# Kernel tuning notes

Measured on AMD Instinct MI355X. Metric: run time of the kernel, lower is better.

The kernel has to match this reference:

```python
import jax, jax.numpy as jnp
import numpy as np

B, LS, LL = 1024, 128, 2048
E, VOCAB = 16, 160000
NH, KD = 8, 6
LSH_DIM, TOPK = 16, 48
D_ITEM = 3 * E  # 48
EPS = 1e-3  # keras LayerNormalization default epsilon


def setup_inputs() -> dict:
    key = jax.random.key(0)
    ks = iter(jax.random.split(key, 64))
    def nk():
        return next(ks)
    def ids(shape):
        return jax.random.randint(nk(), shape, 0, VOCAB, dtype=jnp.int32)
    inp = {}
    for n in ['uid', 'utag1', 'utag2', 'utag3', 'utag4',
              'label_goods_ids', 'label_shop_ids', 'label_cate_ids']:
        inp[n] = ids((B,))
    for n in ['shortterm_goods_ids', 'shortterm_shop_ids', 'shortterm_cate_ids']:
        inp[n] = ids((B, LS))
    for n in ['longterm_goods_ids', 'longterm_shop_ids', 'longterm_cate_ids']:
        inp[n] = ids((B, LL))
    def rn(shape, s=0.05):
        return (jax.random.normal(nk(), shape) * s).astype(jnp.float32)
    inp['emb_table'] = rn((VOCAB, E))
    inp['H'] = rn((D_ITEM, LSH_DIM), 1.0)  # non-trainable random projection
    for p in ('s', 'l'):
        inp[p + 'Wq'] = rn((D_ITEM, NH, KD)); inp[p + 'bq'] = jnp.zeros((NH, KD), jnp.float32)
        inp[p + 'Wk'] = rn((D_ITEM, NH, KD)); inp[p + 'bk'] = jnp.zeros((NH, KD), jnp.float32)
        inp[p + 'Wv'] = rn((D_ITEM, NH, KD)); inp[p + 'bv'] = jnp.zeros((NH, KD), jnp.float32)
        inp[p + 'Wo'] = rn((NH, KD, D_ITEM)); inp[p + 'bo'] = jnp.zeros((D_ITEM,), jnp.float32)
    Din = D_ITEM + 5 * E + D_ITEM + D_ITEM  # 224
    inp['W1'] = rn((Din, 200)); inp['b1'] = jnp.zeros((200,), jnp.float32)
    inp['g1'] = jnp.ones((200,), jnp.float32); inp['be1'] = jnp.zeros((200,), jnp.float32)
    inp['W2'] = rn((200, 80)); inp['b2'] = jnp.zeros((80,), jnp.float32)
    inp['g2'] = jnp.ones((80,), jnp.float32); inp['be2'] = jnp.zeros((80,), jnp.float32)
    inp['W3'] = rn((80, 1)); inp['b3'] = jnp.zeros((1,), jnp.float32)
    return inp


def _ln(x, g, b):
    m = jnp.mean(x, axis=-1, keepdims=True)
    v = jnp.mean((x - m) ** 2, axis=-1, keepdims=True)
    return (x - m) * jax.lax.rsqrt(v + EPS) * g + b


def _mha(q, kv, mask3, Wq, bq, Wk, bk, Wv, bv, Wo, bo):
    # q: [B,1,D], kv: [B,K,D], mask3: [B,1,K] float (1=keep)
    qh = jnp.einsum('bqe,ehd->bqhd', q, Wq) + bq
    kh = jnp.einsum('bke,ehd->bkhd', kv, Wk) + bk
    vh = jnp.einsum('bke,ehd->bkhd', kv, Wv) + bv
    sc = jnp.einsum('bqhd,bkhd->bhqk', qh, kh) / jnp.sqrt(jnp.float32(KD))
    sc = sc + (1.0 - mask3[:, None, :, :]) * jnp.float32(-1e9)
    a = jax.nn.softmax(sc, axis=-1)
    o = jnp.einsum('bhqk,bkhd->bqhd', a, vh)
    return jnp.einsum('bqhd,hde->bqe', o, Wo) + bo


def reference(uid, utag1, utag2, utag3, utag4,
              label_goods_ids, label_shop_ids, label_cate_ids,
              shortterm_goods_ids, shortterm_shop_ids, shortterm_cate_ids,
              longterm_goods_ids, longterm_shop_ids, longterm_cate_ids,
              emb_table, H,
              sWq, sbq, sWk, sbk, sWv, sbv, sWo, sbo,
              lWq, lbq, lWk, lbk, lWv, lbv, lWo, lbo,
              W1, b1, g1, be1, W2, b2, g2, be2, W3, b3):
    short_mask = shortterm_goods_ids == 0  # padding_index == 0
    long_mask = longterm_goods_ids == 0

    def stack_embed(lst):
        X = jnp.stack([t if t.ndim == 2 else t[:, None] for t in lst], axis=2)  # [B,L,F]
        Xe = emb_table[X]  # [B,L,F,E]
        return Xe.reshape(Xe.shape[0], Xe.shape[1], -1)

    X_item = stack_embed([label_goods_ids, label_shop_ids, label_cate_ids])  # [B,1,48]
    X_user = stack_embed([uid, utag1, utag2, utag3, utag4])                  # [B,1,80]
    X_short = stack_embed([shortterm_goods_ids, shortterm_shop_ids, shortterm_cate_ids])  # [B,LS,48]
    X_long = stack_embed([longterm_goods_ids, longterm_shop_ids, longterm_cate_ids])      # [B,LL,48]

    # short-term interest
    slen = jnp.sum((~short_mask).astype(jnp.int32), axis=1)
    smask = (jnp.arange(LS)[None, :] < slen[:, None]).astype(jnp.float32)[:, None, :]
    short_int = _mha(X_item, X_short, smask, sWq, sbq, sWk, sbk, sWv, sbv, sWo, sbo)[:, 0]

    # long-term interest: LSH sign-hash hamming top-k retrieval
    series_codes = jnp.sign(jnp.einsum('ble,em->blm', X_long, H))  # [B,LL,16]
    item_codes = jnp.sign(jnp.einsum('ble,em->blm', X_item, H))    # [B,1,16]
    scores = jnp.sum((series_codes == item_codes).astype(jnp.float32), axis=-1)  # [B,LL]
    scores = jnp.where(long_mask, -jnp.inf, scores)
    _, idx = jax.lax.top_k(scores, TOPK)  # descending, padded entries last
    top_emb = jnp.take_along_axis(X_long, idx[:, :, None], axis=1)  # [B,TOPK,48]
    top_mask = jnp.take_along_axis(long_mask, idx, axis=1)
    llen = jnp.sum((~top_mask).astype(jnp.int32), axis=1)
    lmask = (jnp.arange(TOPK)[None, :] < llen[:, None]).astype(jnp.float32)[:, None, :]
    long_int = _mha(X_item, top_emb, lmask, lWq, lbq, lWk, lbk, lWv, lbv, lWo, lbo)[:, 0]

    x = jnp.concatenate([X_item[:, 0], X_user[:, 0], short_int, long_int], axis=1)  # [B,224]
    h1 = jax.nn.relu(_ln(x @ W1 + b1, g1, be1))
    h2 = jax.nn.relu(_ln(h1 @ W2 + b2, g2, be2))
    out = jax.nn.sigmoid(h2 @ W3 + b3)  # [B,1]
    return out
```

## Files before the change

### kernel.cpp

```cpp
#include <hip/hip_runtime.h>
#include <math.h>

#define BB 1024
#define LSx 128
#define LLx 2048
#define TOPKx 48

__global__ __launch_bounds__(256) void k_score(
    const int* __restrict__ lg, const int* __restrict__ lsh, const int* __restrict__ lc,
    const int* __restrict__ ig, const int* __restrict__ ish, const int* __restrict__ ici,
    const float* __restrict__ emb, const float* __restrict__ Hm,
    signed char* __restrict__ gsc)
{
  __shared__ float Xitem[48];
  __shared__ int icode[16];
  const int b = blockIdx.y, tid = threadIdx.x;

  if (tid < 48) {
    const int seg = tid >> 4, e = tid & 15;
    const int id = (seg == 0) ? ig[b] : (seg == 1) ? ish[b] : ici[b];
    Xitem[tid] = emb[(size_t)id * 16 + e];
  }
  __syncthreads();
  if (tid < 16) {
    float dd = 0.f;
    for (int e = 0; e < 48; ++e) dd += Xitem[e] * Hm[e * 16 + tid];
    icode[tid] = (dd > 0.f) ? 1 : (dd < 0.f ? -1 : 0);
  }
  __syncthreads();

  const int l = blockIdx.x * 256 + tid;
  const size_t off = (size_t)b * LLx + l;
  const int gid = lg[off];
  int sc;
  if (gid == 0) {
    sc = -1;
  } else {
    const int sid = lsh[off], cid = lc[off];
    float d[16];
    #pragma unroll
    for (int m = 0; m < 16; ++m) d[m] = 0.f;
    const int ids3[3] = {gid, sid, cid};
    #pragma unroll
    for (int seg = 0; seg < 3; ++seg) {
      const float* row = emb + (size_t)ids3[seg] * 16;
      const float4 r0 = ((const float4*)row)[0];
      const float4 r1 = ((const float4*)row)[1];
      const float4 r2 = ((const float4*)row)[2];
      const float4 r3 = ((const float4*)row)[3];
      const float x[16] = {r0.x, r0.y, r0.z, r0.w, r1.x, r1.y, r1.z, r1.w,
                           r2.x, r2.y, r2.z, r2.w, r3.x, r3.y, r3.z, r3.w};
      const float* hb = Hm + seg * 256;
      #pragma unroll
      for (int i = 0; i < 16; ++i) {
        const float xi = x[i];
        #pragma unroll
        for (int mc = 0; mc < 4; ++mc) {
          const float4 h4 = *(const float4*)(hb + i * 16 + mc * 4);
          d[mc * 4 + 0] += xi * h4.x;
          d[mc * 4 + 1] += xi * h4.y;
          d[mc * 4 + 2] += xi * h4.z;
          d[mc * 4 + 3] += xi * h4.w;
        }
      }
    }
    sc = 0;
    #pragma unroll
    for (int m = 0; m < 16; ++m) {
      const int cs = (d[m] > 0.f) ? 1 : (d[m] < 0.f ? -1 : 0);
      sc += (cs == icode[m]) ? 1 : 0;
    }
  }
  gsc[off] = (signed char)sc;
}

template<int K, int STRIDE, bool IS_LONG>
__global__ __launch_bounds__(128) void k_mha(
    const int* __restrict__ kg, const int* __restrict__ ks, const int* __restrict__ kc,
    const int* __restrict__ ig, const int* __restrict__ ish, const int* __restrict__ ici,
    const float* __restrict__ emb,
    const float* __restrict__ Wq, const float* __restrict__ bq,
    const float* __restrict__ Wk, const float* __restrict__ bk,
    const float* __restrict__ Wv, const float* __restrict__ bv,
    const float* __restrict__ Wo, const float* __restrict__ bo,
    const int* __restrict__ sel,
    float* __restrict__ outv)
{
  __shared__ float Xitem[48];
  __shared__ float qh[48];
  __shared__ __align__(16) float vhs[K][48];
  __shared__ float scs[8][K + 4];
  __shared__ float osm[48];
  __shared__ unsigned char validf[K];
  const int b = blockIdx.x, tid = threadIdx.x;

  if (tid < 48) {
    const int seg = tid >> 4, e = tid & 15;
    const int id = (seg == 0) ? ig[b] : (seg == 1) ? ish[b] : ici[b];
    Xitem[tid] = emb[(size_t)id * 16 + e];
  }
  __syncthreads();
  if (tid < 48) {
    float a = bq[tid];
    for (int e = 0; e < 48; ++e) a += Xitem[e] * Wq[e * 48 + tid];
    qh[tid] = a;
  }

  int gid = 0, sid = 0, cid = 0;
  if (tid < K) {
    const int pos = IS_LONG ? sel[b * TOPKx + tid] : tid;
    const size_t off = (size_t)b * STRIDE + pos;
    gid = kg[off]; sid = ks[off]; cid = kc[off];
  }
  const int nval = __syncthreads_count((tid < K) && (gid != 0));

  if (tid < K) {
    validf[tid] = IS_LONG ? (unsigned char)(gid != 0) : (unsigned char)(tid < nval);
    float kh[48], vh[48];
    #pragma unroll
    for (int j = 0; j < 48; ++j) { kh[j] = bk[j]; vh[j] = bv[j]; }
    const int ids3[3] = {gid, sid, cid};
    #pragma unroll
    for (int seg = 0; seg < 3; ++seg) {
      const float* row = emb + (size_t)ids3[seg] * 16;
      #pragma unroll
      for (int i4 = 0; i4 < 4; ++i4) {
        const float4 xv = ((const float4*)row)[i4];
        const float xs[4] = {xv.x, xv.y, xv.z, xv.w};
        #pragma unroll
        for (int c = 0; c < 4; ++c) {
          const int e = seg * 16 + i4 * 4 + c;
          const float* wkr = Wk + e * 48;
          const float* wvr = Wv + e * 48;
          const float xe = xs[c];
          #pragma unroll
          for (int j = 0; j < 48; ++j) {
            kh[j] += xe * wkr[j];
            vh[j] += xe * wvr[j];
          }
        }
      }
    }
    #pragma unroll
    for (int h = 0; h < 8; ++h) {
      float s = 0.f;
      #pragma unroll
      for (int d = 0; d < 6; ++d) s += qh[h * 6 + d] * kh[h * 6 + d];
      scs[h][tid] = s * 0.40824829046386301637f;
    }
    #pragma unroll
    for (int j = 0; j < 48; ++j) vhs[tid][j] = vh[j];
  }
  __syncthreads();

  {
    const int h = tid >> 4, l16 = tid & 15;
    float amax = -INFINITY;
    for (int k = l16; k < K; k += 16) if (validf[k]) amax = fmaxf(amax, scs[h][k]);
    #pragma unroll
    for (int m = 1; m < 16; m <<= 1) amax = fmaxf(amax, __shfl_xor(amax, m, 16));
    if (nval == 0) {
      for (int k = l16; k < K; k += 16) scs[h][k] = 1.0f / (float)K;
    } else {
      float ssum = 0.f;
      for (int k = l16; k < K; k += 16) {
        const float ev = validf[k] ? expf(scs[h][k] - amax) : 0.f;
        scs[h][k] = ev;
        ssum += ev;
      }
      #pragma unroll
      for (int m = 1; m < 16; m <<= 1) ssum += __shfl_xor(ssum, m, 16);
      const float inv = 1.0f / ssum;
      for (int k = l16; k < K; k += 16) scs[h][k] *= inv;
    }
  }
  __syncthreads();

  if (tid < 48) {
    const int h = tid / 6;
    float a = 0.f;
    for (int k = 0; k < K; ++k) a += scs[h][k] * vhs[k][tid];
    osm[tid] = a;
  }
  __syncthreads();
  if (tid < 48) {
    float r = bo[tid];
    for (int j = 0; j < 48; ++j) r += osm[j] * Wo[j * 48 + tid];
    outv[b * 48 + tid] = r;
  }
}

__global__ __launch_bounds__(256) void k_mha_long(
    const int* __restrict__ kg, const int* __restrict__ ks, const int* __restrict__ kc,
    const int* __restrict__ ig, const int* __restrict__ ish, const int* __restrict__ ici,
    const float* __restrict__ emb,
    const float* __restrict__ Wq, const float* __restrict__ bq,
    const float* __restrict__ Wk, const float* __restrict__ bk,
    const float* __restrict__ Wv, const float* __restrict__ bv,
    const float* __restrict__ Wo, const float* __restrict__ bo,
    const signed char* __restrict__ gsc,
    float* __restrict__ outv)
{
  __shared__ int hist[18];
  __shared__ int cnt_above;
  __shared__ int wsum[4];
  __shared__ int selsh[TOPKx];
  __shared__ float Xitem[48];
  __shared__ float qh[48];
  __shared__ __align__(16) float vhs[TOPKx][48];
  __shared__ float scs[8][TOPKx + 4];
  __shared__ float osm[48];
  __shared__ unsigned char validf[TOPKx];
  const int b = blockIdx.x, tid = threadIdx.x;

  const int2 myv = ((const int2*)(gsc + (size_t)b * LLx))[tid];
  signed char loc[8];
  *(int2*)loc = myv;

  if (tid < 18) hist[tid] = 0;
  if (tid == 0) cnt_above = 0;
  if (tid < 48) {
    const int seg = tid >> 4, e = tid & 15;
    const int id = (seg == 0) ? ig[b] : (seg == 1) ? ish[b] : ici[b];
    Xitem[tid] = emb[(size_t)id * 16 + e];
  }
  __syncthreads();

  #pragma unroll
  for (int j = 0; j < 8; ++j) atomicAdd(&hist[(int)loc[j] + 1], 1);
  if (tid < 48) {
    float a = bq[tid];
    for (int e = 0; e < 48; ++e) a += Xitem[e] * Wq[e * 48 + tid];
    qh[tid] = a;
  }
  __syncthreads();

  int above = 0, tval = -1, need = 0;
  for (int s = 16; s >= -1; --s) {
    const int c = hist[s + 1];
    if (above + c >= TOPKx) { tval = s; need = TOPKx - above; break; }
    above += c;
  }

  const int base_l = tid * (LLx / 256);
  int cnt = 0;
  #pragma unroll
  for (int j = 0; j < 8; ++j) cnt += ((int)loc[j] == tval) ? 1 : 0;
  int v = cnt;
  const int lane = tid & 63, wave = tid >> 6;
  #pragma unroll
  for (int o = 1; o < 64; o <<= 1) {
    const int u = __shfl_up(v, o, 64);
    if (lane >= o) v += u;
  }
  if (lane == 63) wsum[wave] = v;
  __syncthreads();
  int rank = v - cnt;
  for (int w = 0; w < wave; ++w) rank += wsum[w];

  #pragma unroll
  for (int j = 0; j < 8; ++j) {
    const int l = base_l + j;
    const int s = (int)loc[j];
    if (s > tval) {
      const int slot = atomicAdd(&cnt_above, 1);
      selsh[slot] = l;
    } else if (s == tval) {
      if (rank < need) selsh[above + rank] = l;
      ++rank;
    }
  }
  __syncthreads();

  int gid = 0, sid = 0, cid = 0;
  if (tid < TOPKx) {
    const int pos = selsh[tid];
    const size_t off = (size_t)b * LLx + pos;
    gid = kg[off]; sid = ks[off]; cid = kc[off];
  }
  const int nval = __syncthreads_count((tid < TOPKx) && (gid != 0));

  if (tid < TOPKx) {
    validf[tid] = (unsigned char)(gid != 0);
    float kh[48], vh[48];
    #pragma unroll
    for (int j = 0; j < 48; ++j) { kh[j] = bk[j]; vh[j] = bv[j]; }
    const int ids3[3] = {gid, sid, cid};
    #pragma unroll
    for (int seg = 0; seg < 3; ++seg) {
      const float* row = emb + (size_t)ids3[seg] * 16;
      #pragma unroll
      for (int i4 = 0; i4 < 4; ++i4) {
        const float4 xv = ((const float4*)row)[i4];
        const float xs[4] = {xv.x, xv.y, xv.z, xv.w};
        #pragma unroll
        for (int c = 0; c < 4; ++c) {
          const int e = seg * 16 + i4 * 4 + c;
          const float* wkr = Wk + e * 48;
          const float* wvr = Wv + e * 48;
          const float xe = xs[c];
          #pragma unroll
          for (int j = 0; j < 48; ++j) {
            kh[j] += xe * wkr[j];
            vh[j] += xe * wvr[j];
          }
        }
      }
    }
    #pragma unroll
    for (int h = 0; h < 8; ++h) {
      float s = 0.f;
      #pragma unroll
      for (int d = 0; d < 6; ++d) s += qh[h * 6 + d] * kh[h * 6 + d];
      scs[h][tid] = s * 0.40824829046386301637f;
    }
    #pragma unroll
    for (int j = 0; j < 48; ++j) vhs[tid][j] = vh[j];
  }
  __syncthreads();

  if (tid < 128) {
    const int h = tid >> 4, l16 = tid & 15;
    float amax = -INFINITY;
    for (int k = l16; k < TOPKx; k += 16) if (validf[k]) amax = fmaxf(amax, scs[h][k]);
    #pragma unroll
    for (int m = 1; m < 16; m <<= 1) amax = fmaxf(amax, __shfl_xor(amax, m, 16));
    if (nval == 0) {
      for (int k = l16; k < TOPKx; k += 16) scs[h][k] = 1.0f / (float)TOPKx;
    } else {
      float ssum = 0.f;
      for (int k = l16; k < TOPKx; k += 16) {
        const float ev = validf[k] ? expf(scs[h][k] - amax) : 0.f;
        scs[h][k] = ev;
        ssum += ev;
      }
      #pragma unroll
      for (int m = 1; m < 16; m <<= 1) ssum += __shfl_xor(ssum, m, 16);
      const float inv = 1.0f / ssum;
      for (int k = l16; k < TOPKx; k += 16) scs[h][k] *= inv;
    }
  }
  __syncthreads();

  if (tid < 48) {
    const int h = tid / 6;
    float a = 0.f;
    for (int k = 0; k < TOPKx; ++k) a += scs[h][k] * vhs[k][tid];
    osm[tid] = a;
  }
  __syncthreads();
  if (tid < 48) {
    float r = bo[tid];
    for (int j = 0; j < 48; ++j) r += osm[j] * Wo[j * 48 + tid];
    outv[b * 48 + tid] = r;
  }
}

__device__ __forceinline__ float block_sum256(float v, float* red) {
  #pragma unroll
  for (int m = 32; m >= 1; m >>= 1) v += __shfl_xor(v, m, 64);
  const int lane = threadIdx.x & 63, wave = threadIdx.x >> 6;
  if (lane == 0) red[wave] = v;
  __syncthreads();
  const float t = red[0] + red[1] + red[2] + red[3];
  __syncthreads();
  return t;
}

__global__ __launch_bounds__(256) void k_mlp(
    const int* __restrict__ uid, const int* __restrict__ u1, const int* __restrict__ u2,
    const int* __restrict__ u3, const int* __restrict__ u4,
    const int* __restrict__ ig, const int* __restrict__ ish, const int* __restrict__ ici,
    const float* __restrict__ emb,
    const float* __restrict__ sint, const float* __restrict__ lint,
    const float* __restrict__ W1, const float* __restrict__ b1,
    const float* __restrict__ g1, const float* __restrict__ be1,
    const float* __restrict__ W2, const float* __restrict__ b2,
    const float* __restrict__ g2, const float* __restrict__ be2,
    const float* __restrict__ W3, const float* __restrict__ b3,
    float* __restrict__ out)
{
  __shared__ __align__(16) float x[224];
  __shared__ __align__(16) float h1[200];
  __shared__ float h2[80];
  __shared__ float red[4];
  const int b = blockIdx.x, tid = threadIdx.x;

  if (tid < 128) {
    const int e = tid & 15;
    int id;
    if (tid < 48) {
      const int seg = tid >> 4;
      id = (seg == 0) ? ig[b] : (seg == 1) ? ish[b] : ici[b];
    } else {
      const int f = (tid - 48) >> 4;
      id = (f == 0) ? uid[b] : (f == 1) ? u1[b] : (f == 2) ? u2[b] : (f == 3) ? u3[b] : u4[b];
    }
    x[tid] = emb[(size_t)id * 16 + e];
  } else if (tid < 176) {
    x[tid] = sint[b * 48 + (tid - 128)];
  } else if (tid < 224) {
    x[tid] = lint[b * 48 + (tid - 176)];
  }
  __syncthreads();

  float v = 0.f;
  if (tid < 200) {
    v = b1[tid];
    for (int i4 = 0; i4 < 56; ++i4) {
      const float4 xv = *(const float4*)(x + i4 * 4);
      const float* w = W1 + i4 * 4 * 200 + tid;
      v += xv.x * w[0];
      v += xv.y * w[200];
      v += xv.z * w[400];
      v += xv.w * w[600];
    }
  }
  const float mean1 = block_sum256((tid < 200) ? v : 0.f, red) * (1.0f / 200.0f);
  const float dv = (tid < 200) ? (v - mean1) : 0.f;
  const float var1 = block_sum256(dv * dv, red) * (1.0f / 200.0f);
  if (tid < 200) {
    const float y = (v - mean1) * rsqrtf(var1 + 1e-3f) * g1[tid] + be1[tid];
    h1[tid] = fmaxf(y, 0.f);
  }
  __syncthreads();

  float v2 = 0.f;
  if (tid < 80) {
    v2 = b2[tid];
    for (int i4 = 0; i4 < 50; ++i4) {
      const float4 xv = *(const float4*)(h1 + i4 * 4);
      const float* w = W2 + i4 * 4 * 80 + tid;
      v2 += xv.x * w[0];
      v2 += xv.y * w[80];
      v2 += xv.z * w[160];
      v2 += xv.w * w[240];
    }
  }
  const float mean2 = block_sum256((tid < 80) ? v2 : 0.f, red) * (1.0f / 80.0f);
  const float dv2 = (tid < 80) ? (v2 - mean2) : 0.f;
  const float var2 = block_sum256(dv2 * dv2, red) * (1.0f / 80.0f);
  if (tid < 80) {
    const float y = (v2 - mean2) * rsqrtf(var2 + 1e-3f) * g2[tid] + be2[tid];
    h2[tid] = fmaxf(y, 0.f);
  }
  __syncthreads();

  const float p = (tid < 80) ? h2[tid] * W3[tid] : 0.f;
  const float z = block_sum256(p, red);
  if (tid == 0) {
    out[b] = 1.0f / (1.0f + expf(-(z + b3[0])));
  }
}

extern "C" void kernel_launch(void* const* d_in, const int* in_sizes, int n_in,
                              void* d_out, int out_size, void* d_ws, size_t ws_size,
                              hipStream_t stream) {
  (void)in_sizes; (void)n_in; (void)out_size; (void)ws_size;
  const int* uid = (const int*)d_in[0];
  const int* u1  = (const int*)d_in[1];
  const int* u2  = (const int*)d_in[2];
  const int* u3  = (const int*)d_in[3];
  const int* u4  = (const int*)d_in[4];
  const int* ig  = (const int*)d_in[5];
  const int* ish = (const int*)d_in[6];
  const int* ici = (const int*)d_in[7];
  const int* sg  = (const int*)d_in[8];
  const int* ss  = (const int*)d_in[9];
  const int* scd = (const int*)d_in[10];
  const int* lg  = (const int*)d_in[11];
  const int* ls  = (const int*)d_in[12];
  const int* lcd = (const int*)d_in[13];
  const float* emb = (const float*)d_in[14];
  const float* Hm  = (const float*)d_in[15];
  const float* sWq = (const float*)d_in[16];
  const float* sbq = (const float*)d_in[17];
  const float* sWk = (const float*)d_in[18];
  const float* sbk = (const float*)d_in[19];
  const float* sWv = (const float*)d_in[20];
  const float* sbv = (const float*)d_in[21];
  const float* sWo = (const float*)d_in[22];
  const float* sbo = (const float*)d_in[23];
  const float* lWq = (const float*)d_in[24];
  const float* lbq = (const float*)d_in[25];
  const float* lWk = (const float*)d_in[26];
  const float* lbk = (const float*)d_in[27];
  const float* lWv = (const float*)d_in[28];
  const float* lbv = (const float*)d_in[29];
  const float* lWo = (const float*)d_in[30];
  const float* lbo = (const float*)d_in[31];
  const float* W1 = (const float*)d_in[32];
  const float* b1 = (const float*)d_in[33];
  const float* g1 = (const float*)d_in[34];
  const float* be1 = (const float*)d_in[35];
  const float* W2 = (const float*)d_in[36];
  const float* b2 = (const float*)d_in[37];
  const float* g2 = (const float*)d_in[38];
  const float* be2 = (const float*)d_in[39];
  const float* W3 = (const float*)d_in[40];
  const float* b3 = (const float*)d_in[41];
  float* out = (float*)d_out;

  signed char* gsc = (signed char*)d_ws;
  float* sint = (float*)((char*)d_ws + (size_t)BB * LLx);
  float* lint = sint + BB * 48;

  k_score<<<dim3(LLx / 256, BB), dim3(256), 0, stream>>>(
      lg, ls, lcd, ig, ish, ici, emb, Hm, gsc);
  k_mha<128, 128, false><<<dim3(BB), dim3(128), 0, stream>>>(
      sg, ss, scd, ig, ish, ici, emb,
      sWq, sbq, sWk, sbk, sWv, sbv, sWo, sbo, (const int*)nullptr, sint);
  k_mha_long<<<dim3(BB), dim3(256), 0, stream>>>(
      lg, ls, lcd, ig, ish, ici, emb,
      lWq, lbq, lWk, lbk, lWv, lbv, lWo, lbo, gsc, lint);
  k_mlp<<<dim3(BB), dim3(256), 0, stream>>>(
      uid, u1, u2, u3, u4, ig, ish, ici, emb,
      sint, lint, W1, b1, g1, be1, W2, b2, g2, be2, W3, b3, out);
}
```

Measured before the change: 352.4 us.

## Split LSH score computation across four lanes per long-sequence position

```diff
diff --git a/kernel.cpp b/kernel.cpp
--- a/kernel.cpp
+++ b/kernel.cpp
@@ -13,7 +13,7 @@
     signed char* __restrict__ gsc)
 {
   __shared__ float Xitem[48];
-  __shared__ int icode[16];
+  __shared__ __align__(16) int icode[16];
   const int b = blockIdx.y, tid = threadIdx.x;
 
   if (tid < 48) {
@@ -29,49 +29,50 @@
   }
   __syncthreads();
 
-  const int l = blockIdx.x * 256 + tid;
+  const int p = tid >> 2;
+  const int q = tid & 3;
+  const int l = (blockIdx.x << 6) | p;
   const size_t off = (size_t)b * LLx + l;
   const int gid = lg[off];
-  int sc;
-  if (gid == 0) {
-    sc = -1;
-  } else {
+
+  int sc = -1;
+  if (gid != 0) {
     const int sid = lsh[off], cid = lc[off];
-    float d[16];
-    #pragma unroll
-    for (int m = 0; m < 16; ++m) d[m] = 0.f;
-    const int ids3[3] = {gid, sid, cid};
-    #pragma unroll
-    for (int seg = 0; seg < 3; ++seg) {
-      const float* row = emb + (size_t)ids3[seg] * 16;
-      const float4 r0 = ((const float4*)row)[0];
-      const float4 r1 = ((const float4*)row)[1];
-      const float4 r2 = ((const float4*)row)[2];
-      const float4 r3 = ((const float4*)row)[3];
-      const float x[16] = {r0.x, r0.y, r0.z, r0.w, r1.x, r1.y, r1.z, r1.w,
-                           r2.x, r2.y, r2.z, r2.w, r3.x, r3.y, r3.z, r3.w};
-      const float* hb = Hm + seg * 256;
-      #pragma unroll
-      for (int i = 0; i < 16; ++i) {
-        const float xi = x[i];
-        #pragma unroll
-        for (int mc = 0; mc < 4; ++mc) {
-          const float4 h4 = *(const float4*)(hb + i * 16 + mc * 4);
-          d[mc * 4 + 0] += xi * h4.x;
-          d[mc * 4 + 1] += xi * h4.y;
-          d[mc * 4 + 2] += xi * h4.z;
-          d[mc * 4 + 3] += xi * h4.w;
-        }
+    const float4 xq0 = *(const float4*)(emb + (size_t)gid * 16 + q * 4);
+    const float4 xq1 = *(const float4*)(emb + (size_t)sid * 16 + q * 4);
+    const float4 xq2 = *(const float4*)(emb + (size_t)cid * 16 + q * 4);
+    float d0 = 0.f, d1 = 0.f, d2 = 0.f, d3 = 0.f;
+    const float* hq = Hm + q * 4;
+
+    #define SCORE_SEG(XQ, S)                                                   \
+      {                                                                        \
+        const float xs_[4] = {XQ.x, XQ.y, XQ.z, XQ.w};                         \
+        _Pragma("unroll")                                                      \
+        for (int i = 0; i < 16; ++i) {                                         \
+          const float xi = __shfl(xs_[i & 3], i >> 2, 4);                      \
+          const float4 h4 = *(const float4*)(hq + ((S) * 16 + i) * 16);        \
+          d0 += xi * h4.x;                                                     \
+          d1 += xi * h4.y;                                                     \
+          d2 += xi * h4.z;                                                     \
+          d3 += xi * h4.w;                                                     \
+        }                                                                      \
       }
-    }
-    sc = 0;
-    #pragma unroll
-    for (int m = 0; m < 16; ++m) {
-      const int cs = (d[m] > 0.f) ? 1 : (d[m] < 0.f ? -1 : 0);
-      sc += (cs == icode[m]) ? 1 : 0;
-    }
-  }
-  gsc[off] = (signed char)sc;
+    SCORE_SEG(xq0, 0)
+    SCORE_SEG(xq1, 1)
+    SCORE_SEG(xq2, 2)
+    #undef SCORE_SEG
+
+    const int4 ic = *(const int4*)(icode + q * 4);
+    int part = 0;
+    part += (((d0 > 0.f) ? 1 : (d0 < 0.f ? -1 : 0)) == ic.x) ? 1 : 0;
+    part += (((d1 > 0.f) ? 1 : (d1 < 0.f ? -1 : 0)) == ic.y) ? 1 : 0;
+    part += (((d2 > 0.f) ? 1 : (d2 < 0.f ? -1 : 0)) == ic.z) ? 1 : 0;
+    part += (((d3 > 0.f) ? 1 : (d3 < 0.f ? -1 : 0)) == ic.w) ? 1 : 0;
+    part += __shfl_xor(part, 1, 4);
+    part += __shfl_xor(part, 2, 4);
+    sc = part;
+  }
+  if (q == 0) gsc[off] = (signed char)sc;
 }
 
 template<int K, int STRIDE, bool IS_LONG>
@@ -505,7 +506,7 @@
   float* sint = (float*)((char*)d_ws + (size_t)BB * LLx);
   float* lint = sint + BB * 48;
 
-  k_score<<<dim3(LLx / 256, BB), dim3(256), 0, stream>>>(
+  k_score<<<dim3(LLx / 64, BB), dim3(256), 0, stream>>>(
       lg, ls, lcd, ig, ish, ici, emb, Hm, gsc);
   k_mha<128, 128, false><<<dim3(BB), dim3(128), 0, stream>>>(
       sg, ss, scd, ig, ish, ici, emb,
```

New measurement: 522.0 us. 48.1% more time.

## Stage embedding gathers cooperatively through swizzled shared memory in LSH scoring kernel

Applied to the files above, without the earlier changes.

```diff
diff --git a/kernel.cpp b/kernel.cpp
--- a/kernel.cpp
+++ b/kernel.cpp
@@ -6,7 +6,7 @@
 #define LLx 2048
 #define TOPKx 48
 
-__global__ __launch_bounds__(256) void k_score(
+__global__ __launch_bounds__(256, 8) void k_score(
     const int* __restrict__ lg, const int* __restrict__ lsh, const int* __restrict__ lc,
     const int* __restrict__ ig, const int* __restrict__ ish, const int* __restrict__ ici,
     const float* __restrict__ emb, const float* __restrict__ Hm,
@@ -14,7 +14,12 @@
 {
   __shared__ float Xitem[48];
   __shared__ int icode[16];
+  __shared__ float4 xsh[256][4];
   const int b = blockIdx.y, tid = threadIdx.x;
+
+  const int l = blockIdx.x * 256 + tid;
+  const size_t off = (size_t)b * LLx + l;
+  const int gid = lg[off];
 
   if (tid < 48) {
     const int seg = tid >> 4, e = tid & 15;
@@ -27,29 +32,34 @@
     for (int e = 0; e < 48; ++e) dd += Xitem[e] * Hm[e * 16 + tid];
     icode[tid] = (dd > 0.f) ? 1 : (dd < 0.f ? -1 : 0);
   }
-  __syncthreads();
-
-  const int l = blockIdx.x * 256 + tid;
-  const size_t off = (size_t)b * LLx + l;
-  const int gid = lg[off];
-  int sc;
-  if (gid == 0) {
-    sc = -1;
-  } else {
-    const int sid = lsh[off], cid = lc[off];
-    float d[16];
-    #pragma unroll
-    for (int m = 0; m < 16; ++m) d[m] = 0.f;
-    const int ids3[3] = {gid, sid, cid};
-    #pragma unroll
-    for (int seg = 0; seg < 3; ++seg) {
-      const float* row = emb + (size_t)ids3[seg] * 16;
-      const float4 r0 = ((const float4*)row)[0];
-      const float4 r1 = ((const float4*)row)[1];
-      const float4 r2 = ((const float4*)row)[2];
-      const float4 r3 = ((const float4*)row)[3];
-      const float x[16] = {r0.x, r0.y, r0.z, r0.w, r1.x, r1.y, r1.z, r1.w,
-                           r2.x, r2.y, r2.z, r2.w, r3.x, r3.y, r3.z, r3.w};
+
+  float d[16];
+  #pragma unroll
+  for (int m = 0; m < 16; ++m) d[m] = 0.f;
+
+  const int srow = tid >> 2;
+  const int q = tid & 3;
+  const size_t bbase = (size_t)b * LLx + (size_t)blockIdx.x * 256;
+
+  #pragma unroll
+  for (int seg = 0; seg < 3; ++seg) {
+    const int* idarr = (seg == 0) ? lg : (seg == 1) ? lsh : lc;
+    #pragma unroll
+    for (int jj = 0; jj < 4; ++jj) {
+      const int pos = jj * 64 + srow;
+      const int id = idarr[bbase + pos];
+      const float4 v = *(const float4*)(emb + (size_t)id * 16 + q * 4);
+      xsh[pos][q ^ ((pos >> 1) & 3)] = v;
+    }
+    __syncthreads();
+    if (gid != 0) {
+      float x[16];
+      #pragma unroll
+      for (int qq = 0; qq < 4; ++qq) {
+        const float4 r = xsh[tid][qq ^ ((tid >> 1) & 3)];
+        x[qq * 4 + 0] = r.x; x[qq * 4 + 1] = r.y;
+        x[qq * 4 + 2] = r.z; x[qq * 4 + 3] = r.w;
+      }
       const float* hb = Hm + seg * 256;
       #pragma unroll
       for (int i = 0; i < 16; ++i) {
@@ -64,6 +74,11 @@
         }
       }
     }
+    if (seg < 2) __syncthreads();
+  }
+
+  int sc = -1;
+  if (gid != 0) {
     sc = 0;
     #pragma unroll
     for (int m = 0; m < 16; ++m) {
```

Result: no change. 354.2 us (+0.5%).
